# Kernel optimization log

Measured on AMD Instinct MI355X. Metric: run time of the kernel, lower is better.

Reference implementation:

```python
import jax, jax.numpy as jnp
import numpy as np

MULTI_INFER_NUM = 8
D_EMBED = 128
N_LAYERS = 2
T, B = 2048, 32


def setup_inputs() -> dict:
    key = jax.random.key(0)
    k1, k2, k3, k4 = jax.random.split(key, 4)
    positions = jax.random.randint(k1, (T, B), 0, 16, dtype=jnp.int64)
    outputs = jax.random.normal(k2, (T, B, D_EMBED), dtype=jnp.float32)
    # 4 LinearTransferFeatures per layer (self_forget, logit, logit_forget, out_forget)
    Ws = jax.random.normal(k3, (N_LAYERS, 4, MULTI_INFER_NUM + 1, D_EMBED, D_EMBED), dtype=jnp.float32) * 0.05
    bs = jax.random.normal(k4, (N_LAYERS, 4, MULTI_INFER_NUM + 1, D_EMBED), dtype=jnp.float32) * 0.05
    return {"positions": positions, "outputs": outputs, "Ws": Ws, "bs": bs}


def _linear(x, onehot, W, b):
    # x: [t,b,d]; onehot: [t,b,e]; W: [e,d,f]; b: [e,d]
    # Equivalent to gathering W[r_pos] ([t,b,d,f]) then einsum('ibde,ibd->ibe'),
    # but computed as per-expert GEMMs + one-hot combine (grouped-GEMM form).
    y_all = jnp.einsum('tbd,edf->tbef', x, W)      # per-expert outputs
    y = jnp.einsum('tbef,tbe->tbf', y_all, onehot)  # select token's expert
    return y + jnp.einsum('tbe,ed->tbd', onehot, b)


def reference(positions, outputs, Ws, bs):
    m = Ws.shape[2] - 1  # multi_infer_num
    r_pos = jnp.where(positions < m, positions, m)
    onehot = jax.nn.one_hot(r_pos, m + 1, dtype=outputs.dtype)
    x = outputs
    for l in range(Ws.shape[0]):
        self_forget = _linear(x, onehot, Ws[l, 0], bs[l, 0])
        logit = _linear(x, onehot, Ws[l, 1], bs[l, 1])
        logit_forget = _linear(x, onehot, Ws[l, 2], bs[l, 2])
        out_forget = _linear(x, onehot, Ws[l, 3], bs[l, 3])
        new_res = x * jax.nn.sigmoid(self_forget) + jnp.tanh(logit) * jax.nn.sigmoid(logit_forget)
        x = jnp.tanh(new_res) * jax.nn.sigmoid(out_forget)
    return x
```

## Files before the change

kernel.cpp:

```cpp
#include <hip/hip_runtime.h>
#include <hip/hip_fp16.h>
#include <stdint.h>

#define TOKENS 65536
#define D      128
#define NEXP   9
#define MT     32
#define MAXTILES (TOKENS / MT + NEXP)
#define NHB    256

typedef _Float16 f16;
typedef _Float16 f16x8  __attribute__((ext_vector_type(8)));
typedef float    f32x4  __attribute__((ext_vector_type(4)));
typedef uint32_t u32;
typedef uint16_t u16;

#define WI_CNT      64
#define ECAP_SMALL  8192
#define ECAP_BIG    49152
#define PERM_U16S   (8 * ECAP_SMALL + ECAP_BIG)
#define WS_PERM_OFF 2048
#define WS_WF_OFF   (WS_PERM_OFF + PERM_U16S * 2)

#define EBASE(E) ((E) < 8 ? ((E) << 13) : 65536)

#define LOG2E  1.44269504f

__global__ void k_pre(const float* __restrict__ Ws, const int* __restrict__ pos,
                      int* __restrict__ wsI, u16* __restrict__ perm16,
                      f16* __restrict__ Wf) {
  const int tid = threadIdx.x;
  if (blockIdx.x >= 256) {
    const int bx  = blockIdx.x - 256;
    const int mat = bx >> 2;
    const int q   = bx & 3;
    const float* src = Ws + (size_t)mat * (D * D);
    f16* dst = Wf + (size_t)mat * (D * D);
#pragma unroll
    for (int p = 0; p < 2; ++p) {
      int cc = q * 512 + p * 256 + tid;
      int ln = cc & 63;
      int kb = (cc >> 6) & 3;
      int c  = cc >> 8;
      int quad = ln >> 4, n = ln & 15;
      int f  = c * 16 + n;
      int d0 = kb * 32 + quad * 8;
      f16x8 w;
#pragma unroll
      for (int i = 0; i < 8; ++i) w[i] = (f16)src[(d0 + i) * D + f];
      *(f16x8*)(dst + cc * 8) = w;
    }
  } else {
    const int b = blockIdx.x;
    const int lane = tid & 63, w = tid >> 6;
    __shared__ int waveCnt[4][NEXP];
    __shared__ int waveBase[4][NEXP];
    __shared__ int blockBase[NEXP];

    int e = pos[b * 256 + tid]; e = e < 8 ? e : 8;
    int myRank = 0;
#pragma unroll
    for (int ee = 0; ee < NEXP; ++ee) {
      unsigned long long m = __ballot(e == ee);
      if (e == ee) myRank = __popcll(m & ((1ull << lane) - 1ull));
      if (lane == 0) waveCnt[w][ee] = __popcll(m);
    }
    __syncthreads();
    if (tid < NEXP) {
      int s = 0;
#pragma unroll
      for (int w2 = 0; w2 < 4; ++w2) { waveBase[w2][tid] = s; s += waveCnt[w2][tid]; }
      blockBase[tid] = atomicAdd(&wsI[WI_CNT + tid * 32], s);
    }
    __syncthreads();
    perm16[EBASE(e) + blockBase[e] + waveBase[w][e] + myRank] = (u16)(b * 256 + tid);
  }
}

__launch_bounds__(256, 4)
__global__ void k_main(const float* __restrict__ xin, const float* __restrict__ bsPtr,
                       const int* __restrict__ wsI, const u16* __restrict__ perm16,
                       const f16* __restrict__ Wf, float* __restrict__ outPtr) {
  __shared__ __attribute__((aligned(16))) f16 Ash[MT][136];
  __shared__ __attribute__((aligned(16))) float Osh[MT][132];
  __shared__ int s_tok[MT];

  const int tid = threadIdx.x;
  const int bid = blockIdx.x;

  int e = 0, tileOffE = 0, cntE = 0, to = 0;
#pragma unroll
  for (int ee = 0; ee < NEXP; ee++) {
    int c = wsI[WI_CNT + ee * 32];
    if (to <= bid) { e = ee; tileOffE = to; cntE = c; }
    to += (c + MT - 1) >> 5;
  }
  if (bid >= to) return;
  const int tokStart   = (bid - tileOffE) * MT;
  const int rowsValid  = min(MT, cntE - tokStart);
  const int permBase   = EBASE(e) + tokStart;

  const int lane = tid & 63;
  const int n    = lane & 15;
  const int quad = lane >> 4;
  const int cBase = (tid >> 6) * 2;
  const int vlane = lane * 8;
  const f16* We = Wf + (size_t)e * 16384;
  const int f0 = cBase * 16 + n;

  f16x8 aF0[4], aF1[4];
  f16x8 b0[4], b1[4];

#define PFB(BUF, LL, CC, JJ)                                                   \
  do {                                                                         \
    if ((LL) < 2) {                                                            \
      const f16* _p = We + ((LL) * 4 + (JJ)) * 147456 + (CC) * 2048 + vlane;   \
      _Pragma("unroll")                                                        \
      for (int _kb = 0; _kb < 4; ++_kb)                                        \
        BUF[_kb] = *(const f16x8*)(_p + _kb * 512);                            \
    }                                                                          \
  } while (0)

#define LOAD_AF()                                                              \
  do {                                                                         \
    _Pragma("unroll")                                                          \
    for (int _kb = 0; _kb < 4; ++_kb) {                                        \
      aF0[_kb] = *(const f16x8*)&Ash[n][_kb * 32 + quad * 8];                  \
      aF1[_kb] = *(const f16x8*)&Ash[16 + n][_kb * 32 + quad * 8];             \
    }                                                                          \
  } while (0)

#define MFMA2(G, BUF, BV)                                                      \
  do {                                                                         \
    f32x4 _x = {(BV), (BV), (BV), (BV)};                                       \
    f32x4 _y = _x;                                                             \
    _Pragma("unroll")                                                          \
    for (int _kb = 0; _kb < 4; ++_kb) {                                        \
      _x = __builtin_amdgcn_mfma_f32_16x16x32_f16(aF0[_kb], BUF[_kb], _x, 0, 0, 0); \
      _y = __builtin_amdgcn_mfma_f32_16x16x32_f16(aF1[_kb], BUF[_kb], _y, 0, 0, 0); \
    }                                                                          \
    acc[G][0] = _x; acc[G][1] = _y;                                            \
  } while (0)

  PFB(b0, 0, cBase, 0);
  PFB(b1, 0, cBase, 1);

  float bias[2][2][4];
#pragma unroll
  for (int l = 0; l < 2; ++l)
#pragma unroll
    for (int ci = 0; ci < 2; ++ci)
#pragma unroll
      for (int j = 0; j < 4; ++j)
        bias[l][ci][j] = bsPtr[((l * 4 + j) * NEXP + e) * D + f0 + ci * 16];

  {
    int m = tid >> 3, h = tid & 7;
    bool valid = (m < rowsValid);
    int tok = 0;
    if (valid) tok = (int)perm16[permBase + m];
    if (h == 0) s_tok[m] = valid ? tok : -1;
    const float4* src = (const float4*)(xin + (size_t)tok * D + h * 16);
    f16* drow = &Ash[m][h * 16];
#pragma unroll
    for (int i = 0; i < 2; i++) {
      float4 a = make_float4(0.f, 0.f, 0.f, 0.f), b2v = a;
      if (valid) { a = src[2 * i]; b2v = src[2 * i + 1]; }
      f16x8 wv;
      wv[0] = (f16)a.x;   wv[1] = (f16)a.y;   wv[2] = (f16)a.z;   wv[3] = (f16)a.w;
      wv[4] = (f16)b2v.x; wv[5] = (f16)b2v.y; wv[6] = (f16)b2v.z; wv[7] = (f16)b2v.w;
      *(f16x8*)&drow[i * 8] = wv;
    }
  }
  __syncthreads();
  LOAD_AF();
  __syncthreads();

#define STAGE(L, CI, NL, NC)                                                   \
  do {                                                                         \
    const int cc = cBase + (CI);                                               \
    const int f = f0 + (CI) * 16;                                              \
    f32x4 acc[4][2];                                                           \
    PFB(b1, L, cc, 1);  MFMA2(0, b0, bias[L][CI][0]);                          \
    PFB(b0, L, cc, 2);  MFMA2(1, b1, bias[L][CI][1]);                          \
    PFB(b1, L, cc, 3);  MFMA2(2, b0, bias[L][CI][2]);                          \
    PFB(b0, NL, NC, 0); MFMA2(3, b1, bias[L][CI][3]);                          \
    \
    float xv[2][4];                                                            \
    _Pragma("unroll")                                                          \
    for (int s = 0; s < 2; s++)                                                \
      _Pragma("unroll")                                                        \
      for (int r = 0; r < 4; r++)                                              \
        xv[s][r] = (float)Ash[s * 16 + quad * 4 + r][f];                       \
    _Pragma("unroll")                                                          \
    for (int s = 0; s < 2; s++) {                                              \
      _Pragma("unroll")                                                        \
      for (int r = 0; r < 4; r++) {                                            \
        int m = s * 16 + quad * 4 + r;              \
        float sf = acc[0][s][r];                    \
        float lg = acc[1][s][r];                                               \
        float lf = acc[2][s][r];                                               \
        float of = acc[3][s][r];                                               \
         \
        float Ea = __builtin_amdgcn_exp2f(-LOG2E * sf);                        \
        float Eb = __builtin_amdgcn_exp2f((2.0f * LOG2E) * lg);                \
        float Ec = __builtin_amdgcn_exp2f(-LOG2E * lf);                        \
        float d1 = 1.0f + Ea, d2 = Eb + 1.0f, d3 = 1.0f + Ec;                  \
        float p23 = d2 * d3;                                                   \
        float nr = (xv[s][r] * p23 + (d2 - 2.0f) * d1) *                       \
                   __builtin_amdgcn_rcpf(d1 * p23);                            \
        float Ed = __builtin_amdgcn_exp2f((2.0f * LOG2E) * nr);                \
        float Ee = __builtin_amdgcn_exp2f(-LOG2E * of);                        \
        float xn = (Ed - 1.0f) * __builtin_amdgcn_rcpf((Ed + 1.0f) * (1.0f + Ee)); \
        if ((L) == 0) {                                                        \
          Ash[m][f] = (f16)xn;                   \
        } else {                                                               \
          Osh[m][f] = xn;                         \
        }                                                                      \
      }                                                                        \
    }                                                                          \
  } while (0)

  STAGE(0, 0, 0, cBase + 1);
  STAGE(0, 1, 1, cBase);
  __syncthreads();
  LOAD_AF();
  STAGE(1, 0, 1, cBase + 1);
  STAGE(1, 1, 2, 0);

  __syncthreads();

  {
    const int c4 = tid & 31;
    const int r0 = tid >> 5;
#pragma unroll
    for (int k = 0; k < 4; ++k) {
      int m = r0 + k * 8;
      int tok = s_tok[m];
      if (tok >= 0) {
        float4 v = *(const float4*)&Osh[m][c4 * 4];
        *(float4*)(outPtr + (size_t)tok * D + c4 * 4) = v;
      }
    }
  }
#undef STAGE
#undef MFMA2
#undef LOAD_AF
#undef PFB
}

extern "C" void kernel_launch(void* const* d_in, const int* in_sizes, int n_in,
                              void* d_out, int out_size, void* d_ws, size_t ws_size,
                              hipStream_t stream) {
  const int*   pos = (const int*)d_in[0];
  const float* x   = (const float*)d_in[1];
  const float* Ws  = (const float*)d_in[2];
  const float* bs  = (const float*)d_in[3];
  float* out = (float*)d_out;
  int* wsI = (int*)d_ws;
  u16* perm16 = (u16*)((char*)d_ws + WS_PERM_OFF);
  f16* Wf = (f16*)((char*)d_ws + WS_WF_OFF);

  hipMemsetAsync((char*)d_ws + WI_CNT * 4, 0, NEXP * 32 * 4, stream);
  k_pre <<<544, 256, 0, stream>>>(Ws, pos, wsI, perm16, Wf);
  k_main<<<MAXTILES, 256, 0, stream>>>(x, bs, wsI, perm16, Wf, out);
}
```

Baseline: 129.7 us.

## Double token tile to 64 rows with 8 waves and store outputs directly

The per-expert token tile grows from 32 to 64 rows and the block from 256 to 512 threads. Each group of four waves handles one 32-row half, so both halves share the block's setup and its weight traffic through cache. The Osh shared-memory staging buffer and the final barrier-plus-copy pass are removed; layer-2 results are written straight to global memory through the token permutation. This cuts shared memory use and one synchronization, but the global stores become scalar writes with only partial coalescing. The doubled tile also adds more padding waste in each expert's last tile.

```diff
diff --git a/kernel.cpp b/kernel.cpp
--- a/kernel.cpp
+++ b/kernel.cpp
@@ -5,7 +5,7 @@
 #define TOKENS 65536
 #define D      128
 #define NEXP   9
-#define MT     32
+#define MT     64
 #define MAXTILES (TOKENS / MT + NEXP)
 #define NHB    256
 
@@ -77,12 +77,11 @@
   }
 }
 
-__launch_bounds__(256, 4)
+__launch_bounds__(512, 4)
 __global__ void k_main(const float* __restrict__ xin, const float* __restrict__ bsPtr,
                        const int* __restrict__ wsI, const u16* __restrict__ perm16,
                        const f16* __restrict__ Wf, float* __restrict__ outPtr) {
   __shared__ __attribute__((aligned(16))) f16 Ash[MT][136];
-  __shared__ __attribute__((aligned(16))) float Osh[MT][132];
   __shared__ int s_tok[MT];
 
   const int tid = threadIdx.x;
@@ -93,7 +92,7 @@
   for (int ee = 0; ee < NEXP; ee++) {
     int c = wsI[WI_CNT + ee * 32];
     if (to <= bid) { e = ee; tileOffE = to; cntE = c; }
-    to += (c + MT - 1) >> 5;
+    to += (c + MT - 1) >> 6;
   }
   if (bid >= to) return;
   const int tokStart   = (bid - tileOffE) * MT;
@@ -103,7 +102,9 @@
   const int lane = tid & 63;
   const int n    = lane & 15;
   const int quad = lane >> 4;
-  const int cBase = (tid >> 6) * 2;
+  const int wid  = tid >> 6;
+  const int cBase = (wid & 3) * 2;
+  const int rB    = (wid >> 2) * 32;
   const int vlane = lane * 8;
   const f16* We = Wf + (size_t)e * 16384;
   const int f0 = cBase * 16 + n;
@@ -125,8 +126,8 @@
   do {                                                                         \
     _Pragma("unroll")                                                          \
     for (int _kb = 0; _kb < 4; ++_kb) {                                        \
-      aF0[_kb] = *(const f16x8*)&Ash[n][_kb * 32 + quad * 8];                  \
-      aF1[_kb] = *(const f16x8*)&Ash[16 + n][_kb * 32 + quad * 8];             \
+      aF0[_kb] = *(const f16x8*)&Ash[rB + n][_kb * 32 + quad * 8];             \
+      aF1[_kb] = *(const f16x8*)&Ash[rB + 16 + n][_kb * 32 + quad * 8];        \
     }                                                                          \
   } while (0)
 
@@ -191,12 +192,12 @@
     for (int s = 0; s < 2; s++)                                                \
       _Pragma("unroll")                                                        \
       for (int r = 0; r < 4; r++)                                              \
-        xv[s][r] = (float)Ash[s * 16 + quad * 4 + r][f];                       \
+        xv[s][r] = (float)Ash[rB + s * 16 + quad * 4 + r][f];                  \
     _Pragma("unroll")                                                          \
     for (int s = 0; s < 2; s++) {                                              \
       _Pragma("unroll")                                                        \
       for (int r = 0; r < 4; r++) {                                            \
-        int m = s * 16 + quad * 4 + r;              \
+        int m = rB + s * 16 + quad * 4 + r;         \
         float sf = acc[0][s][r];                    \
         float lg = acc[1][s][r];                                               \
         float lf = acc[2][s][r];                                               \
@@ -215,7 +216,8 @@
         if ((L) == 0) {                                                        \
           Ash[m][f] = (f16)xn;                   \
         } else {                                                               \
-          Osh[m][f] = xn;                         \
+          int tok = s_tok[m];                                                  \
+          if (tok >= 0) outPtr[(size_t)tok * D + f] = xn;                      \
         }                                                                      \
       }                                                                        \
     }                                                                          \
@@ -228,21 +230,6 @@
   STAGE(1, 0, 1, cBase + 1);
   STAGE(1, 1, 2, 0);
 
-  __syncthreads();
-
-  {
-    const int c4 = tid & 31;
-    const int r0 = tid >> 5;
-#pragma unroll
-    for (int k = 0; k < 4; ++k) {
-      int m = r0 + k * 8;
-      int tok = s_tok[m];
-      if (tok >= 0) {
-        float4 v = *(const float4*)&Osh[m][c4 * 4];
-        *(float4*)(outPtr + (size_t)tok * D + c4 * 4) = v;
-      }
-    }
-  }
 #undef STAGE
 #undef MFMA2
 #undef LOAD_AF
@@ -263,5 +250,5 @@
 
   hipMemsetAsync((char*)d_ws + WI_CNT * 4, 0, NEXP * 32 * 4, stream);
   k_pre <<<544, 256, 0, stream>>>(Ws, pos, wsI, perm16, Wf);
-  k_main<<<MAXTILES, 256, 0, stream>>>(x, bs, wsI, perm16, Wf, out);
+  k_main<<<MAXTILES, 512, 0, stream>>>(x, bs, wsI, perm16, Wf, out);
 }
```

New measurement: 130.4 us. Within noise of the previous version (+0.5%).
